# Optimization experiments

Hardware: AMD Instinct MI355X
Metric: run time of the kernel (lower is better)

The kernel has to match this reference:

```python
import jax, jax.numpy as jnp
import numpy as np

N = 50000       # nodes
E = 1600000     # edges (before self loops)
IN = 128        # in_dim
H = 4           # heads
C = 64          # hidden_channels per head
F = H * C       # 256 concat width
OUT = 10
BN_EPS = 1e-5
NEG_SLOPE = 0.2  # PyG GATConv default


def _gat_conv(x, eidx, W, a_src, a_dst, b):
    # x: [N, F_in]; eidx: [2, E2] with self loops (row0=src, row1=dst)
    xw = (x @ W).reshape(N, H, C)                      # [N, H, C]
    s = jnp.einsum('nhc,hc->nh', xw, a_src)            # [N, H]
    d = jnp.einsum('nhc,hc->nh', xw, a_dst)            # [N, H]
    src, dst = eidx[0], eidx[1]
    alpha = jax.nn.leaky_relu(s[src] + d[dst], NEG_SLOPE)   # [E2, H]
    # scatter-softmax over incoming edges of each dst node (numerically stable)
    m = jax.ops.segment_max(alpha, dst, num_segments=N)
    m = jax.lax.stop_gradient(jnp.where(jnp.isfinite(m), m, 0.0))
    ex = jnp.exp(alpha - m[dst])                       # [E2, H]
    denom = jax.ops.segment_sum(ex, dst, num_segments=N)
    w = ex / (denom[dst] + 1e-16)                      # [E2, H]
    # weighted scatter-add aggregation
    out = jax.ops.segment_sum(w[:, :, None] * xw[src], dst, num_segments=N)  # [N,H,C]
    return out.reshape(N, F) + b


def _batchnorm(h, gamma, beta):
    # training-mode batch stats over the node axis
    mu = jnp.mean(h, axis=0)
    var = jnp.var(h, axis=0)
    return (h - mu) * jax.lax.rsqrt(var + BN_EPS) * gamma + beta


def setup_inputs() -> dict:
    key = jax.random.key(0)
    ks = jax.random.split(key, 12)
    sc = 0.05
    x = jax.random.normal(ks[0], (N, IN), jnp.float32)
    edge_index = jax.random.randint(ks[1], (2, E), 0, N, jnp.int64)
    return {
        'x': x,
        'edge_index': edge_index,
        'W1': jax.random.normal(ks[2], (IN, F), jnp.float32) * sc,
        'a_src1': jax.random.normal(ks[3], (H, C), jnp.float32) * sc,
        'a_dst1': jax.random.normal(ks[4], (H, C), jnp.float32) * sc,
        'b1': jnp.zeros((F,), jnp.float32),
        'W2': jax.random.normal(ks[5], (F, F), jnp.float32) * sc,
        'a_src2': jax.random.normal(ks[6], (H, C), jnp.float32) * sc,
        'a_dst2': jax.random.normal(ks[7], (H, C), jnp.float32) * sc,
        'b2': jnp.zeros((F,), jnp.float32),
        'g1': jnp.ones((F,), jnp.float32),
        'be1': jnp.zeros((F,), jnp.float32),
        'g2': jnp.ones((F,), jnp.float32),
        'be2': jnp.zeros((F,), jnp.float32),
        'Wc': jax.random.normal(ks[8], (F, OUT), jnp.float32) * sc,
        'bc': jnp.zeros((OUT,), jnp.float32),
    }


def reference(x, edge_index, W1, a_src1, a_dst1, b1, W2, a_src2, a_dst2, b2,
              g1, be1, g2, be2, Wc, bc):
    # add self loops (PyG GATConv default add_self_loops=True)
    loops = jnp.arange(N, dtype=edge_index.dtype)
    eidx = jnp.concatenate([edge_index, jnp.stack([loops, loops])], axis=1)
    h = jax.nn.relu(_gat_conv(x, eidx, W1, a_src1, a_dst1, b1))
    h = _batchnorm(h, g1, be1)          # dropout(0.2) treated as identity (eval)
    h = jax.nn.relu(_gat_conv(h, eidx, W2, a_src2, a_dst2, b2))
    h = _batchnorm(h, g2, be2)
    out = h @ Wc + bc                   # [N, OUT]
    return out[None]                    # [1, N, OUT]; squeeze(-1) is a no-op for OUT>1
```

## Files before the change

### kernel.cpp

```cpp
#include <hip/hip_runtime.h>

#define N_NODES 50000
#define E_EDGES 1600000
#define E2 (E_EDGES + N_NODES)
#define HEADS 4
#define F 256
#define OUTC 10
#define BN_EPS 1e-5f
#define NEG_SLOPE 0.2f
#define NSLICE 64
#define SB 1024
#define NB ((N_NODES + SB - 1) / SB)

#define NXCD 8
#define NR (N_NODES / NXCD)
#define EPB 2048
#define NCHUNK ((E2 + EPB - 1) / EPB)

#define CXB (N_NODES * 128 / 4 / 256)
#define CWB 128
#define CDB (NXCD * NCHUNK)

static_assert(N_NODES % (4) == 0, "grid_nw exact");
static_assert(N_NODES % NXCD == 0, "ranges exact");

typedef __attribute__((ext_vector_type(8))) short short8;
typedef __attribute__((ext_vector_type(4))) float f32x4;

__device__ __forceinline__ unsigned short f2bf(float f) {
    unsigned int u = __float_as_uint(f);
    unsigned int r = (u + 0x7fffu + ((u >> 16) & 1u)) >> 16;
    return (unsigned short)r;
}
__device__ __forceinline__ float bf2f(unsigned short b) {
    return __uint_as_float(((unsigned int)b) << 16);
}

__global__ __launch_bounds__(256) void mega_prep(
    const float* __restrict__ X, unsigned short* __restrict__ Xb,
    const float* __restrict__ W1, unsigned short* __restrict__ WT,
    const int* __restrict__ eidx, int* __restrict__ deg)
{
    const int b = blockIdx.x;
    const int t = threadIdx.x;
    if (b < CXB) {
        const int i = b * 256 + t;
        float4 v = reinterpret_cast<const float4*>(X)[i];
        ushort4 o = { f2bf(v.x), f2bf(v.y), f2bf(v.z), f2bf(v.w) };
        reinterpret_cast<ushort4*>(Xb)[i] = o;
    } else if (b < CXB + CWB) {
        const int k = b - CXB;
        WT[t * 128 + k] = f2bf(W1[k * 256 + t]);
    } else {
        const int b2 = b - CXB - CWB;
        const int r = b2 & (NXCD - 1);
        const int chunk = b2 >> 3;
        const int lo = r * NR;
        const int base = chunk * EPB;
        for (int i = t; i < EPB; i += 256) {
            const int e = base + i;
            if (e >= E2) break;
            int dst = (e < E_EDGES) ? eidx[E_EDGES + e] : e - E_EDGES;
            if ((unsigned)(dst - lo) >= (unsigned)NR) continue;
            atomicAdd(&deg[dst], 1);
        }
    }
}

__global__ __launch_bounds__(SB) void scan_blocks(
    const int* __restrict__ deg, int* __restrict__ rowptr, int* __restrict__ bsum)
{
    __shared__ int sm[SB];
    const int t = threadIdx.x;
    const int idx = blockIdx.x * SB + t;
    int v = (idx < N_NODES) ? deg[idx] : 0;
    sm[t] = v;
    __syncthreads();
    for (int off = 1; off < SB; off <<= 1) {
        int u = (t >= off) ? sm[t - off] : 0;
        __syncthreads();
        sm[t] += u;
        __syncthreads();
    }
    if (idx < N_NODES) rowptr[idx] = sm[t] - v;
    if (t == SB - 1) bsum[blockIdx.x] = sm[t];
}

__global__ __launch_bounds__(SB) void scan_add2(
    int* __restrict__ rowptr, const int* __restrict__ bsum)
{
    __shared__ int boff_s;
    if (threadIdx.x == 0) {
        int run = 0;
        for (int b = 0; b < (int)blockIdx.x; b++) run += bsum[b];
        boff_s = run;
        if (blockIdx.x == 0) {
            int tot = 0;
            for (int b = 0; b < NB; b++) tot += bsum[b];
            rowptr[N_NODES] = tot;
        }
    }
    __syncthreads();
    const int idx = blockIdx.x * SB + threadIdx.x;
    if (idx < N_NODES) rowptr[idx] += boff_s;
}

__global__ __launch_bounds__(256) void scatter_edges8(
    const int* __restrict__ eidx, const int* __restrict__ rowptr,
    int* __restrict__ cursor, int* __restrict__ esrc)
{
    const int r = blockIdx.x & (NXCD - 1);
    const int chunk = blockIdx.x >> 3;
    const int lo = r * NR;
    const int base = chunk * EPB;
    for (int i = threadIdx.x; i < EPB; i += 256) {
        const int e = base + i;
        if (e >= E2) break;
        int dst = (e < E_EDGES) ? eidx[E_EDGES + e] : e - E_EDGES;
        if ((unsigned)(dst - lo) >= (unsigned)NR) continue;
        int src = (e < E_EDGES) ? eidx[e] : dst;
        int pos = atomicAdd(&cursor[dst], 1);
        esrc[rowptr[dst] + pos] = src;
    }
}

template<int K, bool BROW>
__global__ __launch_bounds__(256) void gemm_sd(
    const unsigned short* __restrict__ A, const unsigned short* __restrict__ BT,
    const float* __restrict__ brow, const float* __restrict__ a_src,
    const float* __restrict__ a_dst, unsigned short* __restrict__ C,
    float* __restrict__ S, float* __restrict__ D)
{
    const int t = threadIdx.x;
    const int wave = t >> 6, lane = t & 63;
    const int lo = lane & 15, hi = lane >> 4;
    const int row0 = blockIdx.x * 64;
    const int nbase = wave * 64;

    int arow[4];
#pragma unroll
    for (int m = 0; m < 4; m++)
        arow[m] = min(row0 + m * 16 + lo, N_NODES - 1);

    f32x4 acc[4][4];
#pragma unroll
    for (int m = 0; m < 4; m++)
#pragma unroll
        for (int n = 0; n < 4; n++)
            acc[m][n] = (f32x4){0.f, 0.f, 0.f, 0.f};

    for (int k0 = 0; k0 < K; k0 += 32) {
        const int kk = k0 + hi * 8;
        short8 af[4], bfr[4];
#pragma unroll
        for (int m = 0; m < 4; m++)
            af[m] = *reinterpret_cast<const short8*>(A + (size_t)arow[m] * K + kk);
#pragma unroll
        for (int n = 0; n < 4; n++)
            bfr[n] = *reinterpret_cast<const short8*>(BT + (size_t)(nbase + n * 16 + lo) * K + kk);
#pragma unroll
        for (int m = 0; m < 4; m++)
#pragma unroll
            for (int n = 0; n < 4; n++)
                acc[m][n] = __builtin_amdgcn_mfma_f32_16x16x32_bf16(
                    af[m], bfr[n], acc[m][n], 0, 0, 0);
    }

    float bb[4], asv[4], adv[4];
#pragma unroll
    for (int n = 0; n < 4; n++) {
        int col = nbase + n * 16 + lo;
        bb[n]  = BROW ? brow[col] : 0.f;
        asv[n] = a_src[col];
        adv[n] = a_dst[col];
    }

#pragma unroll
    for (int m = 0; m < 4; m++) {
#pragma unroll
        for (int i = 0; i < 4; i++) {
            const int row = row0 + m * 16 + hi * 4 + i;
            const bool ok = row < N_NODES;
            float ps = 0.f, pd = 0.f;
#pragma unroll
            for (int n = 0; n < 4; n++) {
                float v = acc[m][n][i] + bb[n];
                ps += v * asv[n];
                pd += v * adv[n];
                if (ok) C[(size_t)row * F + nbase + n * 16 + lo] = f2bf(v);
            }
#pragma unroll
            for (int off = 1; off < 16; off <<= 1) {
                ps += __shfl_xor(ps, off, 64);
                pd += __shfl_xor(pd, off, 64);
            }
            if (lo == 0 && ok) {
                S[row * HEADS + wave] = ps;
                D[row * HEADS + wave] = pd;
            }
        }
    }
}

__global__ __launch_bounds__(256) void gat_aggregate(
    const int* __restrict__ rowptr, const int* __restrict__ esrc,
    const float* __restrict__ S, const float* __restrict__ D,
    const unsigned short* __restrict__ XWb, const float* __restrict__ bias,
    unsigned short* __restrict__ Hb, float* __restrict__ stp)
{
    __shared__ int   sbuf[4][64];
    __shared__ float wbuf[4][64][4];
    __shared__ float red_s[4][F];
    __shared__ float red_q[4][F];
    const int wv   = threadIdx.x >> 6;
    const int lane = threadIdx.x & 63;
    const int dst  = blockIdx.x * 4 + wv;
    const int beg = rowptr[dst], end = rowptr[dst + 1];
    const int h = lane >> 4;
    const float4 d4 = *reinterpret_cast<const float4*>(D + dst * HEADS);

    float ax = 0.f, ay = 0.f, az = 0.f, aw = 0.f, den = 0.f;

    for (int i = beg; i < end; i += 64) {
        const int nb = min(64, end - i);
        const bool valid = (i + lane < end);
        const int mysrc = valid ? esrc[i + lane] : 0;
        float4 w4 = {0.f, 0.f, 0.f, 0.f};
        if (valid) {
            const float4 s4 = *reinterpret_cast<const float4*>(S + mysrc * HEADS);
            float z;
            z = s4.x + d4.x; w4.x = __expf(z > 0.f ? z : NEG_SLOPE * z);
            z = s4.y + d4.y; w4.y = __expf(z > 0.f ? z : NEG_SLOPE * z);
            z = s4.z + d4.z; w4.z = __expf(z > 0.f ? z : NEG_SLOPE * z);
            z = s4.w + d4.w; w4.w = __expf(z > 0.f ? z : NEG_SLOPE * z);
        }
        sbuf[wv][lane] = mysrc;
        *reinterpret_cast<float4*>(&wbuf[wv][lane][0]) = w4;

        int j = 0;
        for (; j + 7 < nb; j += 8) {
            int s0 = sbuf[wv][j + 0], s1 = sbuf[wv][j + 1];
            int s2 = sbuf[wv][j + 2], s3 = sbuf[wv][j + 3];
            int s4i = sbuf[wv][j + 4], s5 = sbuf[wv][j + 5];
            int s6 = sbuf[wv][j + 6], s7 = sbuf[wv][j + 7];
            float w0 = wbuf[wv][j + 0][h], w1 = wbuf[wv][j + 1][h];
            float w2 = wbuf[wv][j + 2][h], w3 = wbuf[wv][j + 3][h];
            float w4f = wbuf[wv][j + 4][h], w5 = wbuf[wv][j + 5][h];
            float w6 = wbuf[wv][j + 6][h], w7 = wbuf[wv][j + 7][h];
            ushort4 x0 = *reinterpret_cast<const ushort4*>(XWb + (size_t)s0 * F + lane * 4);
            ushort4 x1 = *reinterpret_cast<const ushort4*>(XWb + (size_t)s1 * F + lane * 4);
            ushort4 x2 = *reinterpret_cast<const ushort4*>(XWb + (size_t)s2 * F + lane * 4);
            ushort4 x3 = *reinterpret_cast<const ushort4*>(XWb + (size_t)s3 * F + lane * 4);
            ushort4 x4 = *reinterpret_cast<const ushort4*>(XWb + (size_t)s4i * F + lane * 4);
            ushort4 x5 = *reinterpret_cast<const ushort4*>(XWb + (size_t)s5 * F + lane * 4);
            ushort4 x6 = *reinterpret_cast<const ushort4*>(XWb + (size_t)s6 * F + lane * 4);
            ushort4 x7 = *reinterpret_cast<const ushort4*>(XWb + (size_t)s7 * F + lane * 4);
            ax += w0 * bf2f(x0.x) + w1 * bf2f(x1.x) + w2 * bf2f(x2.x) + w3 * bf2f(x3.x)
                + w4f * bf2f(x4.x) + w5 * bf2f(x5.x) + w6 * bf2f(x6.x) + w7 * bf2f(x7.x);
            ay += w0 * bf2f(x0.y) + w1 * bf2f(x1.y) + w2 * bf2f(x2.y) + w3 * bf2f(x3.y)
                + w4f * bf2f(x4.y) + w5 * bf2f(x5.y) + w6 * bf2f(x6.y) + w7 * bf2f(x7.y);
            az += w0 * bf2f(x0.z) + w1 * bf2f(x1.z) + w2 * bf2f(x2.z) + w3 * bf2f(x3.z)
                + w4f * bf2f(x4.z) + w5 * bf2f(x5.z) + w6 * bf2f(x6.z) + w7 * bf2f(x7.z);
            aw += w0 * bf2f(x0.w) + w1 * bf2f(x1.w) + w2 * bf2f(x2.w) + w3 * bf2f(x3.w)
                + w4f * bf2f(x4.w) + w5 * bf2f(x5.w) + w6 * bf2f(x6.w) + w7 * bf2f(x7.w);
            den += ((w0 + w1) + (w2 + w3)) + ((w4f + w5) + (w6 + w7));
        }
        for (; j < nb; j++) {
            int   src = sbuf[wv][j];
            float w = wbuf[wv][j][h];
            ushort4 xv = *reinterpret_cast<const ushort4*>(XWb + (size_t)src * F + lane * 4);
            ax += w * bf2f(xv.x); ay += w * bf2f(xv.y);
            az += w * bf2f(xv.z); aw += w * bf2f(xv.w);
            den += w;
        }
    }

    const float inv = 1.f / (den + 1e-16f);
    float4 bv = *reinterpret_cast<const float4*>(bias + lane * 4);
    float v0 = ax * inv + bv.x, v1 = ay * inv + bv.y;
    float v2 = az * inv + bv.z, v3 = aw * inv + bv.w;
    v0 = v0 > 0.f ? v0 : 0.f; v1 = v1 > 0.f ? v1 : 0.f;
    v2 = v2 > 0.f ? v2 : 0.f; v3 = v3 > 0.f ? v3 : 0.f;
    ushort4 o = { f2bf(v0), f2bf(v1), f2bf(v2), f2bf(v3) };
    *reinterpret_cast<ushort4*>(Hb + (size_t)dst * F + lane * 4) = o;

    f32x4 rs = {v0, v1, v2, v3};
    f32x4 rq = {v0 * v0, v1 * v1, v2 * v2, v3 * v3};
    *reinterpret_cast<f32x4*>(&red_s[wv][lane * 4]) = rs;
    *reinterpret_cast<f32x4*>(&red_q[wv][lane * 4]) = rq;
    __syncthreads();
    const int ch = threadIdx.x;
    float s = (red_s[0][ch] + red_s[1][ch]) + (red_s[2][ch] + red_s[3][ch]);
    float q = (red_q[0][ch] + red_q[1][ch]) + (red_q[2][ch] + red_q[3][ch]);
    float* slice = stp + (size_t)(blockIdx.x & (NSLICE - 1)) * (2 * F);
    atomicAdd(&slice[ch], s);
    atomicAdd(&slice[F + ch], q);
}

__global__ __launch_bounds__(256) void fold1(
    const float* __restrict__ stp, const float* __restrict__ g,
    const float* __restrict__ be, const float* __restrict__ W2,
    unsigned short* __restrict__ WT2b, float* __restrict__ brow)
{
    __shared__ float sc_l[F], sh_l[F];
    const int t = threadIdx.x;
    float s = 0.f, q = 0.f;
    for (int b = 0; b < NSLICE; b++) {
        s += stp[(size_t)b * 2 * F + t];
        q += stp[(size_t)b * 2 * F + F + t];
    }
    const float inv_n = 1.f / (float)N_NODES;
    float mu = s * inv_n;
    float var = q * inv_n - mu * mu;
    float sc = rsqrtf(var + BN_EPS) * g[t];
    sc_l[t] = sc;
    sh_l[t] = be[t] - mu * sc;
    __syncthreads();
    if (blockIdx.x < 32) {
        const int k0 = blockIdx.x * 8;
#pragma unroll
        for (int kk = 0; kk < 8; kk++)
            WT2b[(size_t)t * F + k0 + kk] = f2bf(W2[(size_t)(k0 + kk) * F + t] * sc_l[k0 + kk]);
    } else {
        float acc = 0.f;
        for (int k = 0; k < F; k++)
            acc += sh_l[k] * W2[(size_t)k * F + t];
        brow[t] = acc;
    }
}

__global__ __launch_bounds__(256) void fold_wc(
    const float* __restrict__ stp, const float* __restrict__ g,
    const float* __restrict__ be, const float* __restrict__ Wc,
    const float* __restrict__ bc, float* __restrict__ Wcp, float* __restrict__ bcp)
{
    __shared__ float sc_l[F], sh_l[F];
    __shared__ float red[256][OUTC];
    const int t = threadIdx.x;
    float s = 0.f, q = 0.f;
    for (int b = 0; b < NSLICE; b++) {
        s += stp[(size_t)b * 2 * F + t];
        q += stp[(size_t)b * 2 * F + F + t];
    }
    const float inv_n = 1.f / (float)N_NODES;
    float mu = s * inv_n;
    float var = q * inv_n - mu * mu;
    float sc = rsqrtf(var + BN_EPS) * g[t];
    sc_l[t] = sc;
    sh_l[t] = be[t] - mu * sc;
    const float sh_t = be[t] - mu * sc;
#pragma unroll
    for (int o = 0; o < OUTC; o++) {
        float wv = Wc[t * OUTC + o];
        Wcp[t * OUTC + o] = wv * sc;
        red[t][o] = sh_t * wv;
    }
    __syncthreads();
    for (int off = 128; off > 0; off >>= 1) {
        if (t < off) {
#pragma unroll
            for (int o = 0; o < OUTC; o++)
                red[t][o] += red[t + off][o];
        }
        __syncthreads();
    }
    if (t < OUTC) bcp[t] = bc[t] + red[0][t];
}

__global__ __launch_bounds__(256) void classifier(
    const unsigned short* __restrict__ Hb, const float* __restrict__ Wcp,
    const float* __restrict__ bcp, float* __restrict__ out)
{
    __shared__ float wls[F][OUTC + 1];
    const int t = threadIdx.x;
    for (int i = t; i < F * OUTC; i += 256)
        wls[i / OUTC][i % OUTC] = Wcp[i];
    __syncthreads();

    const int wave = t >> 6, lane = t & 63;
    const int n = blockIdx.x * 4 + wave;
    if (n >= N_NODES) return;

    float v[4];
#pragma unroll
    for (int j = 0; j < 4; j++)
        v[j] = bf2f(Hb[(size_t)n * F + j * 64 + lane]);

    float acc[OUTC];
#pragma unroll
    for (int o = 0; o < OUTC; o++) acc[o] = 0.f;
#pragma unroll
    for (int j = 0; j < 4; j++)
#pragma unroll
        for (int o = 0; o < OUTC; o++)
            acc[o] += v[j] * wls[j * 64 + lane][o];

#pragma unroll
    for (int off = 32; off > 0; off >>= 1)
#pragma unroll
        for (int o = 0; o < OUTC; o++)
            acc[o] += __shfl_xor(acc[o], off, 64);

    if (lane == 0) {
#pragma unroll
        for (int o = 0; o < OUTC; o++)
            out[(size_t)n * OUTC + o] = acc[o] + bcp[o];
    }
}

extern "C" void kernel_launch(void* const* d_in, const int* in_sizes, int n_in,
                              void* d_out, int out_size, void* d_ws, size_t ws_size,
                              hipStream_t stream)
{
    const float* x   = (const float*)d_in[0];
    const int*   ei  = (const int*)d_in[1];
    const float* W1  = (const float*)d_in[2];
    const float* as1 = (const float*)d_in[3];
    const float* ad1 = (const float*)d_in[4];
    const float* b1  = (const float*)d_in[5];
    const float* W2  = (const float*)d_in[6];
    const float* as2 = (const float*)d_in[7];
    const float* ad2 = (const float*)d_in[8];
    const float* b2  = (const float*)d_in[9];
    const float* g1  = (const float*)d_in[10];
    const float* be1 = (const float*)d_in[11];
    const float* g2  = (const float*)d_in[12];
    const float* be2 = (const float*)d_in[13];
    const float* Wc  = (const float*)d_in[14];
    const float* bc  = (const float*)d_in[15];
    float* out = (float*)d_out;

    char* w = (char*)d_ws;
    int*   deg   = (int*)w;                      w += (size_t)N_NODES * 4;
    int*   cursor= (int*)w;                      w += (size_t)N_NODES * 4;
    float* stp1  = (float*)w;                    w += (size_t)NSLICE * 2 * F * 4;
    float* stp2  = (float*)w;                    w += (size_t)NSLICE * 2 * F * 4;
    const size_t zero_bytes = (size_t)N_NODES * 8 + (size_t)NSLICE * 2 * F * 8;

    unsigned short* Xb   = (unsigned short*)w;   w += (size_t)N_NODES * 128 * 2;
    unsigned short* XWb  = (unsigned short*)w;   w += (size_t)N_NODES * F * 2;
    unsigned short* Hb   = (unsigned short*)w;   w += (size_t)N_NODES * F * 2;
    unsigned short* WT1b = (unsigned short*)w;   w += 256 * 128 * 2;
    unsigned short* WT2b = (unsigned short*)w;   w += 256 * 256 * 2;
    float* Wcp   = (float*)w;                    w += F * OUTC * 4;
    float* bcp   = (float*)w;                    w += 64;
    float* brow2 = (float*)w;                    w += F * 4;
    float* Sv    = (float*)w;                    w += (size_t)N_NODES * HEADS * 4;
    float* Dv    = (float*)w;                    w += (size_t)N_NODES * HEADS * 4;
    int* rowp    = (int*)w;                      w += (size_t)(N_NODES + 1) * 4;
    int* bsum    = (int*)w;                      w += NB * 4;
    int* esrc    = (int*)w;

    const int grid_nw   = N_NODES / 4;
    const int grid_gemm = (N_NODES + 63) / 64;
    const int grid_prep = CXB + CWB + CDB;
    const int grid_sc   = NXCD * NCHUNK;

    hipMemsetAsync(deg, 0, zero_bytes, stream);
    mega_prep<<<grid_prep, 256, 0, stream>>>(x, Xb, W1, WT1b, ei, deg);
    scan_blocks<<<NB, SB, 0, stream>>>(deg, rowp, bsum);
    scan_add2<<<NB, SB, 0, stream>>>(rowp, bsum);
    scatter_edges8<<<grid_sc, 256, 0, stream>>>(ei, rowp, cursor, esrc);

    gemm_sd<128, false><<<grid_gemm, 256, 0, stream>>>(
        Xb, WT1b, nullptr, as1, ad1, XWb, Sv, Dv);
    gat_aggregate<<<grid_nw, 256, 0, stream>>>(rowp, esrc, Sv, Dv, XWb, b1, Hb, stp1);
    fold1<<<33, 256, 0, stream>>>(stp1, g1, be1, W2, WT2b, brow2);

    gemm_sd<256, true><<<grid_gemm, 256, 0, stream>>>(
        Hb, WT2b, brow2, as2, ad2, XWb, Sv, Dv);
    gat_aggregate<<<grid_nw, 256, 0, stream>>>(rowp, esrc, Sv, Dv, XWb, b2, Hb, stp2);
    fold_wc<<<1, 256, 0, stream>>>(stp2, g2, be2, Wc, bc, Wcp, bcp);

    classifier<<<grid_nw, 256, 0, stream>>>(Hb, Wcp, bcp, out);
}
```

Before: 532.9 us.

## Switch intermediates to fp16 with packed-half aggregation and merge scan kernels

Replaces bf16 storage and MFMA with fp16 throughout, and does the edge aggregation with packed f16x2 multiply-adds using two accumulator sets instead of fp32 scalar FMAs. The aim is to cut ALU and conversion work in the gather loop. It also folds the two-pass prefix scan into one kernel where each block recomputes its own offset by reducing all preceding degrees. The cost is fp16 accumulation of the weighted sums and denominator, which risks precision loss or overflow, since the exp weights are not max-subtracted. The scan merge also adds redundant global reads.

```diff
diff --git a/kernel.cpp b/kernel.cpp
--- a/kernel.cpp
+++ b/kernel.cpp
@@ -21,23 +21,30 @@
 #define CWB 128
 #define CDB (NXCD * NCHUNK)
 
-static_assert(N_NODES % (4) == 0, "grid_nw exact");
+static_assert(N_NODES % 4 == 0, "grid_nw exact");
 static_assert(N_NODES % NXCD == 0, "ranges exact");
 
 typedef __attribute__((ext_vector_type(8))) short short8;
 typedef __attribute__((ext_vector_type(4))) float f32x4;
-
-__device__ __forceinline__ unsigned short f2bf(float f) {
-    unsigned int u = __float_as_uint(f);
-    unsigned int r = (u + 0x7fffu + ((u >> 16) & 1u)) >> 16;
-    return (unsigned short)r;
-}
-__device__ __forceinline__ float bf2f(unsigned short b) {
-    return __uint_as_float(((unsigned int)b) << 16);
+typedef _Float16 f16;
+typedef __attribute__((ext_vector_type(2))) _Float16 f16x2;
+
+__device__ __forceinline__ unsigned short f2h(float f) {
+    f16 h = (f16)f;
+    return __builtin_bit_cast(unsigned short, h);
+}
+__device__ __forceinline__ float h2f(unsigned short b) {
+    return (float)__builtin_bit_cast(f16, b);
+}
+__device__ __forceinline__ f16x2 u2h2(unsigned int u) {
+    return __builtin_bit_cast(f16x2, u);
+}
+__device__ __forceinline__ unsigned int h22u(f16x2 h) {
+    return __builtin_bit_cast(unsigned int, h);
 }
 
 __global__ __launch_bounds__(256) void mega_prep(
-    const float* __restrict__ X, unsigned short* __restrict__ Xb,
+    const float* __restrict__ X, unsigned short* __restrict__ Xh,
     const float* __restrict__ W1, unsigned short* __restrict__ WT,
     const int* __restrict__ eidx, int* __restrict__ deg)
 {
@@ -46,11 +53,11 @@
     if (b < CXB) {
         const int i = b * 256 + t;
         float4 v = reinterpret_cast<const float4*>(X)[i];
-        ushort4 o = { f2bf(v.x), f2bf(v.y), f2bf(v.z), f2bf(v.w) };
-        reinterpret_cast<ushort4*>(Xb)[i] = o;
+        ushort4 o = { f2h(v.x), f2h(v.y), f2h(v.z), f2h(v.w) };
+        reinterpret_cast<ushort4*>(Xh)[i] = o;
     } else if (b < CXB + CWB) {
         const int k = b - CXB;
-        WT[t * 128 + k] = f2bf(W1[k * 256 + t]);
+        WT[t * 128 + k] = f2h(W1[k * 256 + t]);
     } else {
         const int b2 = b - CXB - CWB;
         const int r = b2 & (NXCD - 1);
@@ -67,12 +74,25 @@
     }
 }
 
-__global__ __launch_bounds__(SB) void scan_blocks(
-    const int* __restrict__ deg, int* __restrict__ rowptr, int* __restrict__ bsum)
+__global__ __launch_bounds__(SB) void scan_one(
+    const int* __restrict__ deg, int* __restrict__ rowptr)
 {
     __shared__ int sm[SB];
+    __shared__ int red[SB];
     const int t = threadIdx.x;
     const int idx = blockIdx.x * SB + t;
+
+    int part = 0;
+    const int lim = blockIdx.x * SB;
+    for (int i = t; i < lim; i += SB) part += deg[i];
+    red[t] = part;
+    __syncthreads();
+    for (int off = SB / 2; off > 0; off >>= 1) {
+        if (t < off) red[t] += red[t + off];
+        __syncthreads();
+    }
+    const int boff = red[0];
+
     int v = (idx < N_NODES) ? deg[idx] : 0;
     sm[t] = v;
     __syncthreads();
@@ -82,27 +102,8 @@
         sm[t] += u;
         __syncthreads();
     }
-    if (idx < N_NODES) rowptr[idx] = sm[t] - v;
-    if (t == SB - 1) bsum[blockIdx.x] = sm[t];
-}
-
-__global__ __launch_bounds__(SB) void scan_add2(
-    int* __restrict__ rowptr, const int* __restrict__ bsum)
-{
-    __shared__ int boff_s;
-    if (threadIdx.x == 0) {
-        int run = 0;
-        for (int b = 0; b < (int)blockIdx.x; b++) run += bsum[b];
-        boff_s = run;
-        if (blockIdx.x == 0) {
-            int tot = 0;
-            for (int b = 0; b < NB; b++) tot += bsum[b];
-            rowptr[N_NODES] = tot;
-        }
-    }
-    __syncthreads();
-    const int idx = blockIdx.x * SB + threadIdx.x;
-    if (idx < N_NODES) rowptr[idx] += boff_s;
+    if (idx < N_NODES) rowptr[idx] = boff + sm[t] - v;
+    if (idx == N_NODES - 1) rowptr[N_NODES] = boff + sm[t];
 }
 
 __global__ __launch_bounds__(256) void scatter_edges8(
@@ -162,7 +163,7 @@
         for (int m = 0; m < 4; m++)
 #pragma unroll
             for (int n = 0; n < 4; n++)
-                acc[m][n] = __builtin_amdgcn_mfma_f32_16x16x32_bf16(
+                acc[m][n] = __builtin_amdgcn_mfma_f32_16x16x32_f16(
                     af[m], bfr[n], acc[m][n], 0, 0, 0);
     }
 
@@ -187,7 +188,7 @@
                 float v = acc[m][n][i] + bb[n];
                 ps += v * asv[n];
                 pd += v * adv[n];
-                if (ok) C[(size_t)row * F + nbase + n * 16 + lo] = f2bf(v);
+                if (ok) C[(size_t)row * F + nbase + n * 16 + lo] = f2h(v);
             }
 #pragma unroll
             for (int off = 1; off < 16; off <<= 1) {
@@ -205,11 +206,11 @@
 __global__ __launch_bounds__(256) void gat_aggregate(
     const int* __restrict__ rowptr, const int* __restrict__ esrc,
     const float* __restrict__ S, const float* __restrict__ D,
-    const unsigned short* __restrict__ XWb, const float* __restrict__ bias,
-    unsigned short* __restrict__ Hb, float* __restrict__ stp)
-{
-    __shared__ int   sbuf[4][64];
-    __shared__ float wbuf[4][64][4];
+    const unsigned short* __restrict__ XWh, const float* __restrict__ bias,
+    unsigned short* __restrict__ Hh, float* __restrict__ stp)
+{
+    __shared__ int          sbuf[4][64];
+    __shared__ unsigned int wbuf[4][64][4];
     __shared__ float red_s[4][F];
     __shared__ float red_q[4][F];
     const int wv   = threadIdx.x >> 6;
@@ -219,7 +220,8 @@
     const int h = lane >> 4;
     const float4 d4 = *reinterpret_cast<const float4*>(D + dst * HEADS);
 
-    float ax = 0.f, ay = 0.f, az = 0.f, aw = 0.f, den = 0.f;
+    f16x2 a01a = {0, 0}, a23a = {0, 0}, dna = {0, 0};
+    f16x2 a01b = {0, 0}, a23b = {0, 0}, dnb = {0, 0};
 
     for (int i = beg; i < end; i += 64) {
         const int nb = min(64, end - i);
@@ -235,7 +237,13 @@
             z = s4.w + d4.w; w4.w = __expf(z > 0.f ? z : NEG_SLOPE * z);
         }
         sbuf[wv][lane] = mysrc;
-        *reinterpret_cast<float4*>(&wbuf[wv][lane][0]) = w4;
+        {
+            f16 hx = (f16)w4.x, hy = (f16)w4.y, hz = (f16)w4.z, hw = (f16)w4.w;
+            wbuf[wv][lane][0] = h22u((f16x2){hx, hx});
+            wbuf[wv][lane][1] = h22u((f16x2){hy, hy});
+            wbuf[wv][lane][2] = h22u((f16x2){hz, hz});
+            wbuf[wv][lane][3] = h22u((f16x2){hw, hw});
+        }
 
         int j = 0;
         for (; j + 7 < nb; j += 8) {
@@ -243,46 +251,48 @@
             int s2 = sbuf[wv][j + 2], s3 = sbuf[wv][j + 3];
             int s4i = sbuf[wv][j + 4], s5 = sbuf[wv][j + 5];
             int s6 = sbuf[wv][j + 6], s7 = sbuf[wv][j + 7];
-            float w0 = wbuf[wv][j + 0][h], w1 = wbuf[wv][j + 1][h];
-            float w2 = wbuf[wv][j + 2][h], w3 = wbuf[wv][j + 3][h];
-            float w4f = wbuf[wv][j + 4][h], w5 = wbuf[wv][j + 5][h];
-            float w6 = wbuf[wv][j + 6][h], w7 = wbuf[wv][j + 7][h];
-            ushort4 x0 = *reinterpret_cast<const ushort4*>(XWb + (size_t)s0 * F + lane * 4);
-            ushort4 x1 = *reinterpret_cast<const ushort4*>(XWb + (size_t)s1 * F + lane * 4);
-            ushort4 x2 = *reinterpret_cast<const ushort4*>(XWb + (size_t)s2 * F + lane * 4);
-            ushort4 x3 = *reinterpret_cast<const ushort4*>(XWb + (size_t)s3 * F + lane * 4);
-            ushort4 x4 = *reinterpret_cast<const ushort4*>(XWb + (size_t)s4i * F + lane * 4);
-            ushort4 x5 = *reinterpret_cast<const ushort4*>(XWb + (size_t)s5 * F + lane * 4);
-            ushort4 x6 = *reinterpret_cast<const ushort4*>(XWb + (size_t)s6 * F + lane * 4);
-            ushort4 x7 = *reinterpret_cast<const ushort4*>(XWb + (size_t)s7 * F + lane * 4);
-            ax += w0 * bf2f(x0.x) + w1 * bf2f(x1.x) + w2 * bf2f(x2.x) + w3 * bf2f(x3.x)
-                + w4f * bf2f(x4.x) + w5 * bf2f(x5.x) + w6 * bf2f(x6.x) + w7 * bf2f(x7.x);
-            ay += w0 * bf2f(x0.y) + w1 * bf2f(x1.y) + w2 * bf2f(x2.y) + w3 * bf2f(x3.y)
-                + w4f * bf2f(x4.y) + w5 * bf2f(x5.y) + w6 * bf2f(x6.y) + w7 * bf2f(x7.y);
-            az += w0 * bf2f(x0.z) + w1 * bf2f(x1.z) + w2 * bf2f(x2.z) + w3 * bf2f(x3.z)
-                + w4f * bf2f(x4.z) + w5 * bf2f(x5.z) + w6 * bf2f(x6.z) + w7 * bf2f(x7.z);
-            aw += w0 * bf2f(x0.w) + w1 * bf2f(x1.w) + w2 * bf2f(x2.w) + w3 * bf2f(x3.w)
-                + w4f * bf2f(x4.w) + w5 * bf2f(x5.w) + w6 * bf2f(x6.w) + w7 * bf2f(x7.w);
-            den += ((w0 + w1) + (w2 + w3)) + ((w4f + w5) + (w6 + w7));
+            f16x2 w0 = u2h2(wbuf[wv][j + 0][h]), w1 = u2h2(wbuf[wv][j + 1][h]);
+            f16x2 w2 = u2h2(wbuf[wv][j + 2][h]), w3 = u2h2(wbuf[wv][j + 3][h]);
+            f16x2 w4f = u2h2(wbuf[wv][j + 4][h]), w5 = u2h2(wbuf[wv][j + 5][h]);
+            f16x2 w6 = u2h2(wbuf[wv][j + 6][h]), w7 = u2h2(wbuf[wv][j + 7][h]);
+            uint2 x0 = *reinterpret_cast<const uint2*>(XWh + (size_t)s0 * F + lane * 4);
+            uint2 x1 = *reinterpret_cast<const uint2*>(XWh + (size_t)s1 * F + lane * 4);
+            uint2 x2 = *reinterpret_cast<const uint2*>(XWh + (size_t)s2 * F + lane * 4);
+            uint2 x3 = *reinterpret_cast<const uint2*>(XWh + (size_t)s3 * F + lane * 4);
+            uint2 x4 = *reinterpret_cast<const uint2*>(XWh + (size_t)s4i * F + lane * 4);
+            uint2 x5 = *reinterpret_cast<const uint2*>(XWh + (size_t)s5 * F + lane * 4);
+            uint2 x6 = *reinterpret_cast<const uint2*>(XWh + (size_t)s6 * F + lane * 4);
+            uint2 x7 = *reinterpret_cast<const uint2*>(XWh + (size_t)s7 * F + lane * 4);
+            a01a += w0 * u2h2(x0.x); a23a += w0 * u2h2(x0.y); dna += w0;
+            a01b += w1 * u2h2(x1.x); a23b += w1 * u2h2(x1.y); dnb += w1;
+            a01a += w2 * u2h2(x2.x); a23a += w2 * u2h2(x2.y); dna += w2;
+            a01b += w3 * u2h2(x3.x); a23b += w3 * u2h2(x3.y); dnb += w3;
+            a01a += w4f * u2h2(x4.x); a23a += w4f * u2h2(x4.y); dna += w4f;
+            a01b += w5 * u2h2(x5.x); a23b += w5 * u2h2(x5.y); dnb += w5;
+            a01a += w6 * u2h2(x6.x); a23a += w6 * u2h2(x6.y); dna += w6;
+            a01b += w7 * u2h2(x7.x); a23b += w7 * u2h2(x7.y); dnb += w7;
         }
         for (; j < nb; j++) {
-            int   src = sbuf[wv][j];
-            float w = wbuf[wv][j][h];
-            ushort4 xv = *reinterpret_cast<const ushort4*>(XWb + (size_t)src * F + lane * 4);
-            ax += w * bf2f(xv.x); ay += w * bf2f(xv.y);
-            az += w * bf2f(xv.z); aw += w * bf2f(xv.w);
-            den += w;
-        }
-    }
-
+            int src = sbuf[wv][j];
+            f16x2 wj = u2h2(wbuf[wv][j][h]);
+            uint2 xv = *reinterpret_cast<const uint2*>(XWh + (size_t)src * F + lane * 4);
+            a01a += wj * u2h2(xv.x); a23a += wj * u2h2(xv.y); dna += wj;
+        }
+    }
+
+    const float ax = (float)a01a.x + (float)a01b.x;
+    const float ay = (float)a01a.y + (float)a01b.y;
+    const float az = (float)a23a.x + (float)a23b.x;
+    const float aw = (float)a23a.y + (float)a23b.y;
+    const float den = (float)dna.x + (float)dnb.x;
     const float inv = 1.f / (den + 1e-16f);
     float4 bv = *reinterpret_cast<const float4*>(bias + lane * 4);
     float v0 = ax * inv + bv.x, v1 = ay * inv + bv.y;
     float v2 = az * inv + bv.z, v3 = aw * inv + bv.w;
     v0 = v0 > 0.f ? v0 : 0.f; v1 = v1 > 0.f ? v1 : 0.f;
     v2 = v2 > 0.f ? v2 : 0.f; v3 = v3 > 0.f ? v3 : 0.f;
-    ushort4 o = { f2bf(v0), f2bf(v1), f2bf(v2), f2bf(v3) };
-    *reinterpret_cast<ushort4*>(Hb + (size_t)dst * F + lane * 4) = o;
+    ushort4 o = { f2h(v0), f2h(v1), f2h(v2), f2h(v3) };
+    *reinterpret_cast<ushort4*>(Hh + (size_t)dst * F + lane * 4) = o;
 
     f32x4 rs = {v0, v1, v2, v3};
     f32x4 rq = {v0 * v0, v1 * v1, v2 * v2, v3 * v3};
@@ -300,7 +310,7 @@
 __global__ __launch_bounds__(256) void fold1(
     const float* __restrict__ stp, const float* __restrict__ g,
     const float* __restrict__ be, const float* __restrict__ W2,
-    unsigned short* __restrict__ WT2b, float* __restrict__ brow)
+    unsigned short* __restrict__ WT2h, float* __restrict__ brow)
 {
     __shared__ float sc_l[F], sh_l[F];
     const int t = threadIdx.x;
@@ -320,7 +330,7 @@
         const int k0 = blockIdx.x * 8;
 #pragma unroll
         for (int kk = 0; kk < 8; kk++)
-            WT2b[(size_t)t * F + k0 + kk] = f2bf(W2[(size_t)(k0 + kk) * F + t] * sc_l[k0 + kk]);
+            WT2h[(size_t)t * F + k0 + kk] = f2h(W2[(size_t)(k0 + kk) * F + t] * sc_l[k0 + kk]);
     } else {
         float acc = 0.f;
         for (int k = 0; k < F; k++)
@@ -368,7 +378,7 @@
 }
 
 __global__ __launch_bounds__(256) void classifier(
-    const unsigned short* __restrict__ Hb, const float* __restrict__ Wcp,
+    const unsigned short* __restrict__ Hh, const float* __restrict__ Wcp,
     const float* __restrict__ bcp, float* __restrict__ out)
 {
     __shared__ float wls[F][OUTC + 1];
@@ -384,7 +394,7 @@
     float v[4];
 #pragma unroll
     for (int j = 0; j < 4; j++)
-        v[j] = bf2f(Hb[(size_t)n * F + j * 64 + lane]);
+        v[j] = h2f(Hh[(size_t)n * F + j * 64 + lane]);
 
     float acc[OUTC];
 #pragma unroll
@@ -437,18 +447,17 @@
     float* stp2  = (float*)w;                    w += (size_t)NSLICE * 2 * F * 4;
     const size_t zero_bytes = (size_t)N_NODES * 8 + (size_t)NSLICE * 2 * F * 8;
 
-    unsigned short* Xb   = (unsigned short*)w;   w += (size_t)N_NODES * 128 * 2;
-    unsigned short* XWb  = (unsigned short*)w;   w += (size_t)N_NODES * F * 2;
-    unsigned short* Hb   = (unsigned short*)w;   w += (size_t)N_NODES * F * 2;
-    unsigned short* WT1b = (unsigned short*)w;   w += 256 * 128 * 2;
-    unsigned short* WT2b = (unsigned short*)w;   w += 256 * 256 * 2;
+    unsigned short* Xh   = (unsigned short*)w;   w += (size_t)N_NODES * 128 * 2;
+    unsigned short* XWh  = (unsigned short*)w;   w += (size_t)N_NODES * F * 2;
+    unsigned short* Hh   = (unsigned short*)w;   w += (size_t)N_NODES * F * 2;
+    unsigned short* WT1h = (unsigned short*)w;   w += 256 * 128 * 2;
+    unsigned short* WT2h = (unsigned short*)w;   w += 256 * 256 * 2;
     float* Wcp   = (float*)w;                    w += F * OUTC * 4;
     float* bcp   = (float*)w;                    w += 64;
     float* brow2 = (float*)w;                    w += F * 4;
     float* Sv    = (float*)w;                    w += (size_t)N_NODES * HEADS * 4;
     float* Dv    = (float*)w;                    w += (size_t)N_NODES * HEADS * 4;
     int* rowp    = (int*)w;                      w += (size_t)(N_NODES + 1) * 4;
-    int* bsum    = (int*)w;                      w += NB * 4;
     int* esrc    = (int*)w;
 
     const int grid_nw   = N_NODES / 4;
@@ -457,20 +466,19 @@
     const int grid_sc   = NXCD * NCHUNK;
 
     hipMemsetAsync(deg, 0, zero_bytes, stream);
-    mega_prep<<<grid_prep, 256, 0, stream>>>(x, Xb, W1, WT1b, ei, deg);
-    scan_blocks<<<NB, SB, 0, stream>>>(deg, rowp, bsum);
-    scan_add2<<<NB, SB, 0, stream>>>(rowp, bsum);
+    mega_prep<<<grid_prep, 256, 0, stream>>>(x, Xh, W1, WT1h, ei, deg);
+    scan_one<<<NB, SB, 0, stream>>>(deg, rowp);
     scatter_edges8<<<grid_sc, 256, 0, stream>>>(ei, rowp, cursor, esrc);
 
     gemm_sd<128, false><<<grid_gemm, 256, 0, stream>>>(
-        Xb, WT1b, nullptr, as1, ad1, XWb, Sv, Dv);
-    gat_aggregate<<<grid_nw, 256, 0, stream>>>(rowp, esrc, Sv, Dv, XWb, b1, Hb, stp1);
-    fold1<<<33, 256, 0, stream>>>(stp1, g1, be1, W2, WT2b, brow2);
+        Xh, WT1h, nullptr, as1, ad1, XWh, Sv, Dv);
+    gat_aggregate<<<grid_nw, 256, 0, stream>>>(rowp, esrc, Sv, Dv, XWh, b1, Hh, stp1);
+    fold1<<<33, 256, 0, stream>>>(stp1, g1, be1, W2, WT2h, brow2);
 
     gemm_sd<256, true><<<grid_gemm, 256, 0, stream>>>(
-        Hb, WT2b, brow2, as2, ad2, XWb, Sv, Dv);
-    gat_aggregate<<<grid_nw, 256, 0, stream>>>(rowp, esrc, Sv, Dv, XWb, b2, Hb, stp2);
+        Hh, WT2h, brow2, as2, ad2, XWh, Sv, Dv);
+    gat_aggregate<<<grid_nw, 256, 0, stream>>>(rowp, esrc, Sv, Dv, XWh, b2, Hh, stp2);
     fold_wc<<<1, 256, 0, stream>>>(stp2, g2, be2, Wc, bc, Wcp, bcp);
 
-    classifier<<<grid_nw, 256, 0, stream>>>(Hb, Wcp, bcp, out);
-}
+    classifier<<<grid_nw, 256, 0, stream>>>(Hh, Wcp, bcp, out);
+}
```

Measured after the change: 544.4 us. +2.2%, slower.
